# Performance work log

Measured on AMD Instinct MI355X. Metric: run time of the kernel, lower is better.

The kernel has to match this reference:

```python
import jax, jax.numpy as jnp
import numpy as np

N = 4096        # number of cells (graph nodes)
D = 128         # feature / embedding dim (isize)
NEIGHBOR = 15   # kNN column used for the distance cutoff
GAMMA = 8.0
OMEGA = 0.5


def setup_inputs() -> dict:
    key = jax.random.key(0)
    k = jax.random.split(key, 6)
    features = jax.random.normal(k[0], (N, D), dtype=jnp.float32)
    # sparse binary adjacency (~16 neighbors/node on average), stored dense
    adj = (jax.random.uniform(k[1], (N, N)) < 0.004).astype(jnp.float32)
    # symmetric positive pairwise distances
    d = jax.random.uniform(k[2], (N, N), minval=0.05, maxval=1.0)
    dis = ((d + d.T) * 0.5).astype(jnp.float32)
    scale = 1.0 / np.sqrt(D)
    W0 = (jax.random.normal(k[3], (D, D), dtype=jnp.float32) * scale)
    b0 = jnp.zeros((D,), jnp.float32)
    W1 = (jax.random.normal(k[4], (D, D), dtype=jnp.float32) * scale)
    b1 = jnp.zeros((D,), jnp.float32)
    return {"features": features, "adj": adj, "dis": dis,
            "W0": W0, "b0": b0, "W1": W1, "b1": b1}


def _gcn_layer(h, A, W, b):
    # torch_geometric GCNConv: sym-normalize (A + I), then X' = A_norm @ X @ W + b
    A_hat = A + jnp.eye(A.shape[0], dtype=A.dtype)
    deg = A_hat.sum(axis=1)
    dinv = jnp.where(deg > 0, 1.0 / jnp.sqrt(deg), 0.0)
    A_norm = dinv[:, None] * A_hat * dinv[None, :]
    return A_norm @ (h @ W) + b


def reference(features, adj, dis, W0, b0, W1, b1):
    eps = 1e-8
    # --- buffers precomputed in __init__ of the torch module ---
    d_sorted = jnp.sort(dis, axis=1)
    d_cut = jnp.median(d_sorted[:, NEIGHBOR])
    adj_mask = (dis > 0) & (dis <= d_cut)
    d_scaled = jnp.where(adj_mask, dis, jnp.inf) / d_cut
    s_d = jnp.exp(-GAMMA * d_scaled * d_scaled)   # 1/exp(g*d^2); exp(-inf)=0
    # --- internal_forward: 2 GCN layers on adj.T, relu between ---
    A = adj.T
    h = jax.nn.relu(_gcn_layer(features, A, W0, b0))
    h = _gcn_layer(h, A, W1, b1)
    # --- masked cosine similarity, blend with distance kernel ---
    h_norm = jnp.linalg.norm(h, axis=1, keepdims=True)   # [N,1]
    s1 = (h @ h.T) / (h_norm @ h_norm.T + eps)
    s1 = jnp.maximum(s1, 0.0)
    s = OMEGA * s1 + (1.0 - OMEGA) * s_d
    s = jnp.where(adj_mask, s, 0.0)
    # --- symmetric degree normalization D^{-1/2} S D^{-1/2} ---
    deg = s.sum(axis=1)
    dinv = jnp.where(deg > 0, 1.0 / jnp.sqrt(deg), 0.0)
    s_norm = dinv[:, None] * s * dinv[None, :]
    return s_norm, s
```

## Files before the change

kernel.cpp:

```cpp
#include <hip/hip_runtime.h>

#define N 4096
#define CAP 128

__global__ __launch_bounds__(256) void K1(const float* __restrict__ dis,
                                          const float4* __restrict__ adj4,
                                          const float* __restrict__ X,
                                          const float* __restrict__ W0,
                                          int* __restrict__ cnt1, int* __restrict__ nbr1,
                                          float* __restrict__ r16,
                                          float* __restrict__ cand_d, int* __restrict__ cand_j,
                                          int* __restrict__ cntc, float* __restrict__ Trow,
                                          float* __restrict__ Y0) {
  int b = blockIdx.x, t = threadIdx.x;
  if (b < 4096) {
    __shared__ int lcnt;
    __shared__ float lval[CAP];
    __shared__ int lidx[CAP];
    int row = b;
    const float4* dp = (const float4*)(dis + (size_t)row * N);
    float T = 0.12f;
    int c = 0;
    for (int iter = 0; iter < 24; iter++) {
      if (t == 0) lcnt = 0;
      __syncthreads();
#pragma unroll
      for (int q = 0; q < 4; q++) {
        float4 d = dp[q * 256 + t];
        int jb = (q * 256 + t) << 2;
        if (d.x <= T) { int p = atomicAdd(&lcnt, 1); if (p < CAP) { lval[p] = d.x; lidx[p] = jb + 0; } }
        if (d.y <= T) { int p = atomicAdd(&lcnt, 1); if (p < CAP) { lval[p] = d.y; lidx[p] = jb + 1; } }
        if (d.z <= T) { int p = atomicAdd(&lcnt, 1); if (p < CAP) { lval[p] = d.z; lidx[p] = jb + 2; } }
        if (d.w <= T) { int p = atomicAdd(&lcnt, 1); if (p < CAP) { lval[p] = d.w; lidx[p] = jb + 3; } }
      }
      __syncthreads();
      c = lcnt;
      __syncthreads();
      if (c >= 16 && c <= CAP) break;
      T = (c < 16) ? T * 2.0f : T * 0.5f;
    }
    if (t < c) {
      float v = lval[t];
      int less = 0;
      for (int j = 0; j < c; j++) {
        float u = lval[j];
        less += (u < v) || (u == v && j < t);
      }
      if (less == 15) r16[row] = v;
    }
    for (int k = t; k < c; k += 256) {
      cand_d[row * CAP + k] = lval[k];
      cand_j[row * CAP + k] = lidx[k];
    }
    if (t == 0) { cntc[row] = c; Trow[row] = T; }
  } else if (b < 5120) {
    int chunk = b - 4096;
#pragma unroll
    for (int q = 0; q < 16; q++) {
      int k = chunk * 4096 + q * 256 + t;
      float4 a = adj4[k];
      int base = k << 2;
      int j  = base >> 12;
      int i0 = base & (N - 1);
      if (a.x != 0.f) { int p = atomicAdd(&cnt1[i0 + 0], 1); if (p < CAP) nbr1[(i0 + 0) * CAP + p] = j; }
      if (a.y != 0.f) { int p = atomicAdd(&cnt1[i0 + 1], 1); if (p < CAP) nbr1[(i0 + 1) * CAP + p] = j; }
      if (a.z != 0.f) { int p = atomicAdd(&cnt1[i0 + 2], 1); if (p < CAP) nbr1[(i0 + 2) * CAP + p] = j; }
      if (a.w != 0.f) { int p = atomicAdd(&cnt1[i0 + 3], 1); if (p < CAP) nbr1[(i0 + 3) * CAP + p] = j; }
    }
  } else {
    __shared__ float xs[16][128];
    int g = b - 5120;
    int r0 = g * 16;
    int col = t & 127, half = t >> 7;
#pragma unroll
    for (int q = 0; q < 8; q++) xs[q * 2 + half][col] = X[(size_t)(r0 + q * 2 + half) * 128 + col];
    __syncthreads();
    float acc[8] = {0.f, 0.f, 0.f, 0.f, 0.f, 0.f, 0.f, 0.f};
#pragma unroll 4
    for (int k = 0; k < 128; k++) {
      float wk = W0[k * 128 + col];
#pragma unroll
      for (int r = 0; r < 8; r++) acc[r] = fmaf(xs[half * 8 + r][k], wk, acc[r]);
    }
#pragma unroll
    for (int r = 0; r < 8; r++) Y0[(size_t)(r0 + half * 8 + r) * 128 + col] = acc[r];
  }
}

__global__ __launch_bounds__(256) void K2(const float* __restrict__ r16, float* __restrict__ scal,
                                          const float* __restrict__ Y0, const int* __restrict__ cnt1,
                                          const int* __restrict__ nbr1, const float* __restrict__ b0,
                                          float* __restrict__ h1) {
  int b = blockIdx.x, t = threadIdx.x;
  if (b == 0) {
    __shared__ unsigned int keys[N];
    __shared__ int hist[256];
    __shared__ unsigned int s_prefix;
    __shared__ int s_rank;
#pragma unroll
    for (int q = 0; q < 16; q++) keys[q * 256 + t] = __float_as_uint(r16[q * 256 + t]);
    __syncthreads();
    float res[2];
#pragma unroll
    for (int sel = 0; sel < 2; sel++) {
      if (t == 0) { s_rank = 2047 + sel; s_prefix = 0u; }
      __syncthreads();
      unsigned int mask = 0u;
      for (int shift = 24; shift >= 0; shift -= 8) {
        hist[t] = 0;
        __syncthreads();
        unsigned int prefix = s_prefix;
#pragma unroll
        for (int q = 0; q < 16; q++) {
          unsigned int k = keys[q * 256 + t];
          if ((k & mask) == prefix) atomicAdd(&hist[(k >> shift) & 255], 1);
        }
        __syncthreads();
        if (t == 0) {
          int r = s_rank, acc = 0, bb = 0;
          for (; bb < 256; bb++) { if (acc + hist[bb] > r) break; acc += hist[bb]; }
          s_prefix = prefix | ((unsigned int)bb << shift);
          s_rank = r - acc;
        }
        __syncthreads();
        mask |= (255u << shift);
      }
      res[sel] = __uint_as_float(s_prefix);
      __syncthreads();
    }
    if (t == 0) {
      float dcut = 0.5f * (res[0] + res[1]);
      scal[0] = dcut;
      scal[1] = 1.0f / dcut;
    }
  } else {
    int row = 2 * (b - 1) + (t >> 7);
    int col = t & 127;
    int ci = min(cnt1[row], CAP);
    float dvi = 1.0f / sqrtf((float)ci + 1.0f);
    const int* lst = nbr1 + row * CAP;
    float acc = dvi * Y0[(size_t)row * 128 + col];
    for (int q = 0; q < ci; q++) {
      int j = lst[q];
      float dvj = 1.0f / sqrtf((float)min(cnt1[j], CAP) + 1.0f);
      acc += dvj * Y0[(size_t)j * 128 + col];
    }
    h1[(size_t)row * 128 + col] = fmaxf(dvi * acc + b0[col], 0.0f);
  }
}

__global__ __launch_bounds__(256) void K3(const float* __restrict__ X, const float* __restrict__ W1,
                                          float* __restrict__ Y1) {
  __shared__ float xs[16][128];
  int t = threadIdx.x;
  int r0 = blockIdx.x * 16;
  int col = t & 127, half = t >> 7;
#pragma unroll
  for (int q = 0; q < 8; q++) xs[q * 2 + half][col] = X[(size_t)(r0 + q * 2 + half) * 128 + col];
  __syncthreads();
  float acc[8] = {0.f, 0.f, 0.f, 0.f, 0.f, 0.f, 0.f, 0.f};
#pragma unroll 4
  for (int k = 0; k < 128; k++) {
    float wk = W1[k * 128 + col];
#pragma unroll
    for (int r = 0; r < 8; r++) acc[r] = fmaf(xs[half * 8 + r][k], wk, acc[r]);
  }
#pragma unroll
  for (int r = 0; r < 8; r++) Y1[(size_t)(r0 + half * 8 + r) * 128 + col] = acc[r];
}

__global__ __launch_bounds__(256) void K4(const float* __restrict__ Y1, const int* __restrict__ cnt1,
                                          const int* __restrict__ nbr1, const float* __restrict__ b1,
                                          float* __restrict__ hbuf, float* __restrict__ hnorm) {
  __shared__ float red[4];
  int b = blockIdx.x, t = threadIdx.x;
  int row = 2 * b + (t >> 7);
  int col = t & 127;
  int ci = min(cnt1[row], CAP);
  float dvi = 1.0f / sqrtf((float)ci + 1.0f);
  const int* lst = nbr1 + row * CAP;
  float acc = dvi * Y1[(size_t)row * 128 + col];
  for (int q = 0; q < ci; q++) {
    int j = lst[q];
    float dvj = 1.0f / sqrtf((float)min(cnt1[j], CAP) + 1.0f);
    acc += dvj * Y1[(size_t)j * 128 + col];
  }
  float h = dvi * acc + b1[col];
  hbuf[(size_t)row * 128 + col] = h;
  float ss = h * h;
#pragma unroll
  for (int s = 32; s; s >>= 1) ss += __shfl_xor(ss, s, 64);
  if ((t & 63) == 0) red[t >> 6] = ss;
  __syncthreads();
  if (t == 0)   hnorm[row]     = sqrtf(red[0] + red[1]);
  if (t == 128) hnorm[row]     = sqrtf(red[2] + red[3]);
}

__global__ __launch_bounds__(256) void K5(const float* __restrict__ dis, const float* __restrict__ scal,
                                          const float* __restrict__ cand_d, const int* __restrict__ cand_j,
                                          const int* __restrict__ cntc, const float* __restrict__ Trow,
                                          const float* __restrict__ hbuf, const float* __restrict__ hnorm,
                                          float* __restrict__ vals, int* __restrict__ jdx,
                                          int* __restrict__ cnt2, float* __restrict__ deg) {
  __shared__ float cd[CAP];
  __shared__ int cj[CAP];
  __shared__ float sdv[CAP];
  __shared__ int sj[CAP];
  __shared__ int ccnt, scnt;
  __shared__ float hi[128];
  __shared__ float wred[4];
  int row = blockIdx.x, t = threadIdx.x;
  int wv = t >> 6, ln = t & 63;
  float dcut = scal[0];
  if (t == 0) { scnt = 0; ccnt = 0; }
  if (t < 128) hi[t] = hbuf[(size_t)row * 128 + t];
  __syncthreads();
  int c1;
  if (Trow[row] >= dcut) {
    c1 = cntc[row];
    for (int k = t; k < c1; k += 256) { cd[k] = cand_d[row * CAP + k]; cj[k] = cand_j[row * CAP + k]; }
  } else {
    const float4* dp = (const float4*)(dis + (size_t)row * N);
#pragma unroll
    for (int q = 0; q < 4; q++) {
      float4 d = dp[q * 256 + t];
      int jb = (q * 256 + t) << 2;
      if (d.x <= dcut) { int p = atomicAdd(&ccnt, 1); if (p < CAP) { cd[p] = d.x; cj[p] = jb + 0; } }
      if (d.y <= dcut) { int p = atomicAdd(&ccnt, 1); if (p < CAP) { cd[p] = d.y; cj[p] = jb + 1; } }
      if (d.z <= dcut) { int p = atomicAdd(&ccnt, 1); if (p < CAP) { cd[p] = d.z; cj[p] = jb + 2; } }
      if (d.w <= dcut) { int p = atomicAdd(&ccnt, 1); if (p < CAP) { cd[p] = d.w; cj[p] = jb + 3; } }
    }
    __syncthreads();
    c1 = min(ccnt, CAP);
  }
  __syncthreads();
  if (t < c1) {
    float d = cd[t];
    if (d > 0.f && d <= dcut) {
      float r = d / dcut;
      int p = atomicAdd(&scnt, 1);
      sdv[p] = 0.5f * expf(-8.0f * r * r);
      sj[p] = cj[t];
    }
  }
  __syncthreads();
  int c2 = scnt;
  float ni = hnorm[row];
  float wsum = 0.f;
  for (int idx = wv; idx < c2; idx += 4) {
    int j = sj[idx];
    const float* hj = hbuf + (size_t)j * 128;
    float p = hi[ln] * hj[ln] + hi[ln + 64] * hj[ln + 64];
#pragma unroll
    for (int s = 32; s; s >>= 1) p += __shfl_xor(p, s, 64);
    if (ln == 0) {
      float s1 = fmaxf(p / (ni * hnorm[j] + 1e-8f), 0.f);
      float v = sdv[idx] + 0.5f * s1;
      vals[row * CAP + idx] = v;
      jdx[row * CAP + idx] = j;
      wsum += v;
    }
  }
  if (ln == 0) wred[wv] = wsum;
  __syncthreads();
  if (t == 0) {
    deg[row] = wred[0] + wred[1] + wred[2] + wred[3];
    cnt2[row] = c2;
  }
}

__global__ __launch_bounds__(256) void K6(const float* __restrict__ vals, const int* __restrict__ jdx,
                                          const int* __restrict__ cnt2, const float* __restrict__ deg,
                                          float* __restrict__ s_norm_out, float* __restrict__ s_out) {
  int row = blockIdx.x, t = threadIdx.x;
  float dgi = deg[row];
  float di = (dgi > 0.f) ? (1.0f / sqrtf(dgi)) : 0.f;
  float4 z = {0.f, 0.f, 0.f, 0.f};
  float4* sp = (float4*)(s_out + (size_t)row * N);
  float4* op = (float4*)(s_norm_out + (size_t)row * N);
#pragma unroll
  for (int q = 0; q < 4; q++) {
    sp[q * 256 + t] = z;
    op[q * 256 + t] = z;
  }
  __syncthreads();
  int c2 = cnt2[row];
  if (t < c2) {
    int j = jdx[row * CAP + t];
    float v = vals[row * CAP + t];
    s_out[(size_t)row * N + j] = v;
    float dgj = deg[j];
    float dj = (dgj > 0.f) ? (1.0f / sqrtf(dgj)) : 0.f;
    s_norm_out[(size_t)row * N + j] = di * dj * v;
  }
}

extern "C" void kernel_launch(void* const* d_in, const int* in_sizes, int n_in,
                              void* d_out, int out_size, void* d_ws, size_t ws_size,
                              hipStream_t stream) {
  const float* features = (const float*)d_in[0];
  const float* adj      = (const float*)d_in[1];
  const float* dis      = (const float*)d_in[2];
  const float* W0       = (const float*)d_in[3];
  const float* b0       = (const float*)d_in[4];
  const float* W1       = (const float*)d_in[5];
  const float* b1       = (const float*)d_in[6];
  float* out    = (float*)d_out;
  float* s_half = out + (size_t)N * N;

  char* ws = (char*)d_ws;
  float* r16   = (float*)(ws + 0);
  int*   cnt1  = (int*)  (ws + 16384);
  int*   cntc  = (int*)  (ws + 32768);
  float* Trow  = (float*)(ws + 49152);
  float* deg   = (float*)(ws + 65536);
  int*   cnt2  = (int*)  (ws + 81920);
  float* scal  = (float*)(ws + 98304);
  float* hnorm = (float*)(ws + 114688);
  int*   nbr1  = (int*)  (ws + 131072 + 0 * 2097152);
  float* cand_dv=(float*)(ws + 131072 + 1 * 2097152);
  int*   cand_j= (int*)  (ws + 131072 + 2 * 2097152);
  float* vals  = (float*)(ws + 131072 + 3 * 2097152);
  int*   jdx   = (int*)  (ws + 131072 + 4 * 2097152);
  float* Y0    = (float*)(ws + 131072 + 5 * 2097152);
  float* h1    = (float*)(ws + 131072 + 6 * 2097152);
  float* Y1    = (float*)(ws + 131072 + 7 * 2097152);
  float* hbuf  = (float*)(ws + 131072 + 8 * 2097152);

  hipMemsetAsync(cnt1, 0, N * sizeof(int), stream);

  K1<<<5376, 256, 0, stream>>>(dis, (const float4*)adj, features, W0,
                               cnt1, nbr1, r16, cand_dv, cand_j, cntc, Trow, Y0);
  K2<<<2049, 256, 0, stream>>>(r16, scal, Y0, cnt1, nbr1, b0, h1);
  K3<<<256, 256, 0, stream>>>(h1, W1, Y1);
  K4<<<2048, 256, 0, stream>>>(Y1, cnt1, nbr1, b1, hbuf, hnorm);
  K5<<<4096, 256, 0, stream>>>(dis, scal, cand_dv, cand_j, cntc, Trow,
                               hbuf, hnorm, vals, jdx, cnt2, deg);
  K6<<<4096, 256, 0, stream>>>(vals, jdx, cnt2, deg, out, s_half);
}
```

Baseline: 375.6 us.

## Move output zeroing into first kernel and parallelize median bucket scan

The dense zero-fill of both N×N outputs moves out of the final kernel and into extra blocks of the first kernel, so it overlaps with the distance scan, adjacency build and first matmul. The unnormalized similarity values are now scattered directly from K5, and K6 shrinks to 128 threads that only write the normalized entries. The serial 256-bin scan in the radix select for the median cutoff is replaced by a wave-shuffle prefix sum over all threads. This adds more blocks and more memory traffic to K1, which is already busy, but it removes a separate write-heavy phase from the end of the chain.

```diff
diff --git a/kernel.cpp b/kernel.cpp
--- a/kernel.cpp
+++ b/kernel.cpp
@@ -11,7 +11,8 @@
                                           float* __restrict__ r16,
                                           float* __restrict__ cand_d, int* __restrict__ cand_j,
                                           int* __restrict__ cntc, float* __restrict__ Trow,
-                                          float* __restrict__ Y0) {
+                                          float* __restrict__ Y0,
+                                          float* __restrict__ s_norm_out, float* __restrict__ s_out) {
   int b = blockIdx.x, t = threadIdx.x;
   if (b < 4096) {
     __shared__ int lcnt;
@@ -67,7 +68,7 @@
       if (a.z != 0.f) { int p = atomicAdd(&cnt1[i0 + 2], 1); if (p < CAP) nbr1[(i0 + 2) * CAP + p] = j; }
       if (a.w != 0.f) { int p = atomicAdd(&cnt1[i0 + 3], 1); if (p < CAP) nbr1[(i0 + 3) * CAP + p] = j; }
     }
-  } else {
+  } else if (b < 5376) {
     __shared__ float xs[16][128];
     int g = b - 5120;
     int r0 = g * 16;
@@ -84,6 +85,16 @@
     }
 #pragma unroll
     for (int r = 0; r < 8; r++) Y0[(size_t)(r0 + half * 8 + r) * 128 + col] = acc[r];
+  } else {
+    int row = b - 5376;
+    float4 z = {0.f, 0.f, 0.f, 0.f};
+    float4* sp = (float4*)(s_out + (size_t)row * N);
+    float4* op = (float4*)(s_norm_out + (size_t)row * N);
+#pragma unroll
+    for (int q = 0; q < 4; q++) {
+      sp[q * 256 + t] = z;
+      op[q * 256 + t] = z;
+    }
   }
 }
 
@@ -95,6 +106,7 @@
   if (b == 0) {
     __shared__ unsigned int keys[N];
     __shared__ int hist[256];
+    __shared__ int wsum4[4];
     __shared__ unsigned int s_prefix;
     __shared__ int s_rank;
 #pragma unroll
@@ -116,11 +128,23 @@
           if ((k & mask) == prefix) atomicAdd(&hist[(k >> shift) & 255], 1);
         }
         __syncthreads();
-        if (t == 0) {
-          int r = s_rank, acc = 0, bb = 0;
-          for (; bb < 256; bb++) { if (acc + hist[bb] > r) break; acc += hist[bb]; }
-          s_prefix = prefix | ((unsigned int)bb << shift);
-          s_rank = r - acc;
+        int r = s_rank;
+        int ht = hist[t];
+        int x = ht;
+#pragma unroll
+        for (int s = 1; s < 64; s <<= 1) {
+          int y = __shfl_up(x, s, 64);
+          if ((t & 63) >= s) x += y;
+        }
+        if ((t & 63) == 63) wsum4[t >> 6] = x;
+        __syncthreads();
+        int off = 0;
+#pragma unroll
+        for (int w = 0; w < 4; w++) off += (w < (t >> 6)) ? wsum4[w] : 0;
+        int incl = x + off, excl = incl - ht;
+        if (r >= excl && r < incl) {
+          s_prefix = prefix | ((unsigned int)t << shift);
+          s_rank = r - excl;
         }
         __syncthreads();
         mask |= (255u << shift);
@@ -192,8 +216,8 @@
   for (int s = 32; s; s >>= 1) ss += __shfl_xor(ss, s, 64);
   if ((t & 63) == 0) red[t >> 6] = ss;
   __syncthreads();
-  if (t == 0)   hnorm[row]     = sqrtf(red[0] + red[1]);
-  if (t == 128) hnorm[row]     = sqrtf(red[2] + red[3]);
+  if (t == 0)   hnorm[row] = sqrtf(red[0] + red[1]);
+  if (t == 128) hnorm[row] = sqrtf(red[2] + red[3]);
 }
 
 __global__ __launch_bounds__(256) void K5(const float* __restrict__ dis, const float* __restrict__ scal,
@@ -201,7 +225,8 @@
                                           const int* __restrict__ cntc, const float* __restrict__ Trow,
                                           const float* __restrict__ hbuf, const float* __restrict__ hnorm,
                                           float* __restrict__ vals, int* __restrict__ jdx,
-                                          int* __restrict__ cnt2, float* __restrict__ deg) {
+                                          int* __restrict__ cnt2, float* __restrict__ deg,
+                                          float* __restrict__ s_out) {
   __shared__ float cd[CAP];
   __shared__ int cj[CAP];
   __shared__ float sdv[CAP];
@@ -256,6 +281,7 @@
     if (ln == 0) {
       float s1 = fmaxf(p / (ni * hnorm[j] + 1e-8f), 0.f);
       float v = sdv[idx] + 0.5f * s1;
+      s_out[(size_t)row * N + j] = v;
       vals[row * CAP + idx] = v;
       jdx[row * CAP + idx] = j;
       wsum += v;
@@ -269,26 +295,16 @@
   }
 }
 
-__global__ __launch_bounds__(256) void K6(const float* __restrict__ vals, const int* __restrict__ jdx,
+__global__ __launch_bounds__(128) void K6(const float* __restrict__ vals, const int* __restrict__ jdx,
                                           const int* __restrict__ cnt2, const float* __restrict__ deg,
-                                          float* __restrict__ s_norm_out, float* __restrict__ s_out) {
+                                          float* __restrict__ s_norm_out) {
   int row = blockIdx.x, t = threadIdx.x;
-  float dgi = deg[row];
-  float di = (dgi > 0.f) ? (1.0f / sqrtf(dgi)) : 0.f;
-  float4 z = {0.f, 0.f, 0.f, 0.f};
-  float4* sp = (float4*)(s_out + (size_t)row * N);
-  float4* op = (float4*)(s_norm_out + (size_t)row * N);
-#pragma unroll
-  for (int q = 0; q < 4; q++) {
-    sp[q * 256 + t] = z;
-    op[q * 256 + t] = z;
-  }
-  __syncthreads();
   int c2 = cnt2[row];
   if (t < c2) {
+    float dgi = deg[row];
+    float di = (dgi > 0.f) ? (1.0f / sqrtf(dgi)) : 0.f;
     int j = jdx[row * CAP + t];
     float v = vals[row * CAP + t];
-    s_out[(size_t)row * N + j] = v;
     float dgj = deg[j];
     float dj = (dgj > 0.f) ? (1.0f / sqrtf(dgj)) : 0.f;
     s_norm_out[(size_t)row * N + j] = di * dj * v;
@@ -329,12 +345,13 @@
 
   hipMemsetAsync(cnt1, 0, N * sizeof(int), stream);
 
-  K1<<<5376, 256, 0, stream>>>(dis, (const float4*)adj, features, W0,
-                               cnt1, nbr1, r16, cand_dv, cand_j, cntc, Trow, Y0);
+  K1<<<9472, 256, 0, stream>>>(dis, (const float4*)adj, features, W0,
+                               cnt1, nbr1, r16, cand_dv, cand_j, cntc, Trow, Y0,
+                               out, s_half);
   K2<<<2049, 256, 0, stream>>>(r16, scal, Y0, cnt1, nbr1, b0, h1);
   K3<<<256, 256, 0, stream>>>(h1, W1, Y1);
   K4<<<2048, 256, 0, stream>>>(Y1, cnt1, nbr1, b1, hbuf, hnorm);
   K5<<<4096, 256, 0, stream>>>(dis, scal, cand_dv, cand_j, cntc, Trow,
-                               hbuf, hnorm, vals, jdx, cnt2, deg);
-  K6<<<4096, 256, 0, stream>>>(vals, jdx, cnt2, deg, out, s_half);
-}
+                               hbuf, hnorm, vals, jdx, cnt2, deg, s_half);
+  K6<<<4096, 128, 0, stream>>>(vals, jdx, cnt2, deg, out);
+}
```

After: 337.9 us. 1.11x faster.
